# Optimization experiments

Measured on AMD Instinct MI355X. Metric: run time of the kernel, lower is better.

The kernel has to match this reference:

```python
import jax, jax.numpy as jnp
import numpy as np

B, S, E, H = 2, 2048, 1024, 16
D = E // H  # head dim = 64


def setup_inputs() -> dict:
    key = jax.random.key(0)
    ks = jax.random.split(key, 6)
    x = jax.random.normal(ks[0], (B, S, E), dtype=jnp.float32)
    attn_mask = jax.random.bernoulli(ks[1], 0.1, (B, S, S))  # True = masked
    scale = 1.0 / np.sqrt(E)
    w_kernel = jax.random.normal(ks[2], (E, 3 * E), dtype=jnp.float32) * scale
    w_bias = jax.random.normal(ks[3], (3 * E,), dtype=jnp.float32) * 0.02
    fc_kernel = jax.random.normal(ks[4], (E, E), dtype=jnp.float32) * scale
    fc_bias = jax.random.normal(ks[5], (E,), dtype=jnp.float32) * 0.02
    return {"x": x, "attn_mask": attn_mask, "w_kernel": w_kernel,
            "w_bias": w_bias, "fc_kernel": fc_kernel, "fc_bias": fc_bias}


def reference(x, attn_mask, w_kernel, w_bias, fc_kernel, fc_bias):
    b, s, e = x.shape
    qkv = jnp.einsum("bse,ef->bsf", x, w_kernel) + w_bias  # (B,S,3E)
    q, k, v = jnp.split(qkv, 3, axis=-1)

    def heads(t):  # (B,S,E) -> (B,H,S,D)
        return t.reshape(b, s, H, D).transpose(0, 2, 1, 3)

    q, k, v = heads(q), heads(k), heads(v)
    scores = jnp.einsum("bhqd,bhkd->bhqk", q, k) / jnp.sqrt(jnp.float32(D))
    # faithful quirk: masked positions are filled with 1e-9, not -inf
    scores = jnp.where(attn_mask[:, None, :, :], jnp.float32(1e-9), scores)
    A = jax.nn.softmax(scores, axis=-1)
    out = jnp.einsum("bhqk,bhkd->bhqd", A, v)  # (B,H,S,D)
    out = out.transpose(0, 2, 1, 3).reshape(b, s, e)
    # dropout is identity in eval mode
    return jnp.einsum("bse,ef->bsf", out, fc_kernel) + fc_bias
```

## Files before the change

### kernel.cpp

```cpp
#include <hip/hip_runtime.h>
#include <math.h>

#define BB 2
#define SS 2048
#define EE 1024
#define HH 16

typedef _Float16 f16;
typedef __attribute__((ext_vector_type(8))) _Float16 f16x8;
typedef __attribute__((ext_vector_type(4))) _Float16 f16x4;
typedef __attribute__((ext_vector_type(4))) float f32x4;

__global__ __launch_bounds__(256) void cvt_f32_f16(
    const float* __restrict__ in, f16* __restrict__ out, int n)
{
  int i = (blockIdx.x * 256 + threadIdx.x) * 8;
  if (i >= n) return;
  float4 a = *(const float4*)(in + i);
  float4 b = *(const float4*)(in + i + 4);
  f16x8 o;
  o[0] = (f16)a.x; o[1] = (f16)a.y; o[2] = (f16)a.z; o[3] = (f16)a.w;
  o[4] = (f16)b.x; o[5] = (f16)b.y; o[6] = (f16)b.z; o[7] = (f16)b.w;
  *(f16x8*)(out + i) = o;
}

__global__ __launch_bounds__(256) void transpose_cvt(
    const float* __restrict__ in, f16* __restrict__ out, int K, int N)
{
  __shared__ float T[64][65];
  const int k0 = blockIdx.y * 64, n0 = blockIdx.x * 64;
  const int tr = threadIdx.x >> 4, tc = (threadIdx.x & 15) * 4;
#pragma unroll
  for (int i = 0; i < 4; ++i) {
    int r = tr + i * 16;
    *(float4*)&T[r][tc] = *(const float4*)(in + (size_t)(k0 + r) * N + n0 + tc);
  }
  __syncthreads();
#pragma unroll
  for (int i = 0; i < 4; ++i) {
    int nl = tr + i * 16;
    f16x4 v;
    v[0] = (f16)T[tc + 0][nl];
    v[1] = (f16)T[tc + 1][nl];
    v[2] = (f16)T[tc + 2][nl];
    v[3] = (f16)T[tc + 3][nl];
    *(f16x4*)(out + (size_t)(n0 + nl) * K + k0 + tc) = v;
  }
}

__global__ __launch_bounds__(256) void pack_mask(
    const int* __restrict__ m, unsigned long long* __restrict__ bits)
{
  const int i = blockIdx.x * 256 + threadIdx.x;
  const unsigned long long bal = __ballot(m[i] != 0);
  if ((threadIdx.x & 63) == 0) bits[i >> 6] = bal;
}

__global__ __launch_bounds__(256) void gemm_f16(
    const f16* __restrict__ A, const f16* __restrict__ Bt,
    const float* __restrict__ bias, int M, int N, int K, int mode,
    f16* __restrict__ oQK, f16* __restrict__ oVT, float* __restrict__ oF32)
{
  __shared__ f16 Ah[128][36];
  __shared__ f16 Bh[128][36];

  const int t = threadIdx.x;
  const int l = t & 63, w = t >> 6;
  const int l15 = l & 15, l4 = l >> 4;
  const int wr = w >> 1, wc = w & 1;
  const int n0 = blockIdx.x * 128, m0 = blockIdx.y * 128;

  const int srow = t >> 1, soff = (t & 1) * 16;
  const f16* Ap = A + (size_t)(m0 + srow) * K + soff;
  const f16* Bp = Bt + (size_t)(n0 + srow) * K + soff;

  f32x4 acc[4][4] = {};

  f16x8 ra0 = *(const f16x8*)(Ap);
  f16x8 ra1 = *(const f16x8*)(Ap + 8);
  f16x8 rb0 = *(const f16x8*)(Bp);
  f16x8 rb1 = *(const f16x8*)(Bp + 8);

  for (int k0 = 0; k0 < K; k0 += 32) {
    __syncthreads();
    *(f16x8*)&Ah[srow][soff]     = ra0;
    *(f16x8*)&Ah[srow][soff + 8] = ra1;
    *(f16x8*)&Bh[srow][soff]     = rb0;
    *(f16x8*)&Bh[srow][soff + 8] = rb1;
    __syncthreads();
    if (k0 + 32 < K) {
      ra0 = *(const f16x8*)(Ap + k0 + 32);
      ra1 = *(const f16x8*)(Ap + k0 + 40);
      rb0 = *(const f16x8*)(Bp + k0 + 32);
      rb1 = *(const f16x8*)(Bp + k0 + 40);
    }
    f16x8 af[4], bf[4];
#pragma unroll
    for (int mr = 0; mr < 4; ++mr)
      af[mr] = *(const f16x8*)&Ah[wr * 64 + mr * 16 + l15][l4 * 8];
#pragma unroll
    for (int nr = 0; nr < 4; ++nr)
      bf[nr] = *(const f16x8*)&Bh[wc * 64 + nr * 16 + l15][l4 * 8];
#pragma unroll
    for (int mr = 0; mr < 4; ++mr)
#pragma unroll
      for (int nr = 0; nr < 4; ++nr)
        acc[mr][nr] = __builtin_amdgcn_mfma_f32_16x16x32_f16(
            af[mr], bf[nr], acc[mr][nr], 0, 0, 0);
  }

  if (mode == 1) {
#pragma unroll
    for (int nr = 0; nr < 4; ++nr) {
      const int n = n0 + wc * 64 + nr * 16 + l15;
      const float bv = bias[n];
#pragma unroll
      for (int mr = 0; mr < 4; ++mr)
#pragma unroll
        for (int j = 0; j < 4; ++j) {
          const int m = m0 + wr * 64 + mr * 16 + l4 * 4 + j;
          oF32[(size_t)m * N + n] = acc[mr][nr][j] + bv;
        }
    }
  } else {
#pragma unroll
    for (int nr = 0; nr < 4; ++nr) {
      const int n = n0 + wc * 64 + nr * 16 + l15;
      const float bv = bias[n];
      if (n < 2048) {
#pragma unroll
        for (int mr = 0; mr < 4; ++mr)
#pragma unroll
          for (int j = 0; j < 4; ++j) {
            const int m = m0 + wr * 64 + mr * 16 + l4 * 4 + j;
            oQK[(size_t)m * 2048 + n] = (f16)(acc[mr][nr][j] + bv);
          }
      } else {
        const int hh = (n - 2048) >> 6;
        const int d = (n - 2048) & 63;
#pragma unroll
        for (int mr = 0; mr < 4; ++mr) {
          const int tok0 = m0 + wr * 64 + mr * 16 + l4 * 4;
          const int bq = tok0 >> 11, sq = tok0 & 2047;
          f16x4 v;
          v[0] = (f16)(acc[mr][nr][0] + bv);
          v[1] = (f16)(acc[mr][nr][1] + bv);
          v[2] = (f16)(acc[mr][nr][2] + bv);
          v[3] = (f16)(acc[mr][nr][3] + bv);
          *(f16x4*)(oVT + ((size_t)(bq * 16 + hh) * 64 + d) * SS + sq) = v;
        }
      }
    }
  }
}

__global__ __launch_bounds__(256, 2) void attn_mfma(
    const f16* __restrict__ qkbuf, const f16* __restrict__ vT,
    const unsigned long long* __restrict__ mbits, f16* __restrict__ aout)
{
  __shared__ f16 Kds[2][64 * 64];
  __shared__ f16 Vds[2][64 * 64];

  const int t = threadIdx.x;
  const int w = t >> 6, l = t & 63, l15 = l & 15, l4 = l >> 4;
  const int bh = blockIdx.y, b = bh >> 4, h = bh & 15;
  const int qbase = blockIdx.x * 128 + w * 32;

  f16x8 q00, q01, q10, q11;
  {
    const size_t r0 = (size_t)(b * SS + qbase + l15) * 2048 + h * 64;
    const size_t r1 = (size_t)(b * SS + qbase + 16 + l15) * 2048 + h * 64;
    q00 = *(const f16x8*)(qkbuf + r0 + l4 * 8);
    q01 = *(const f16x8*)(qkbuf + r0 + 32 + l4 * 8);
    q10 = *(const f16x8*)(qkbuf + r1 + l4 * 8);
    q11 = *(const f16x8*)(qkbuf + r1 + 32 + l4 * 8);
  }

  f32x4 accA[4] = {}, accB[4] = {};
  float lsA = 0.f, lsB = 0.f;

  const unsigned long long* mA = mbits + (size_t)(b * SS + qbase + l15) * 32;
  const unsigned long long* mB = mbits + (size_t)(b * SS + qbase + 16 + l15) * 32;

  const int srow = t >> 3;
  const int scb  = (t & 7) * 8;
  const int sws  = (srow & 7) << 3;
  const f16* kb = qkbuf + (size_t)b * SS * 2048 + 1024 + h * 64 + scb;
  const f16* vb = vT + ((size_t)bh * 64 + srow) * SS + scb;

  f16x8 kr0, kr1, vr0, vr1;
#define LOADT(kt)                                                         \
  {                                                                       \
    kr0 = *(const f16x8*)(kb + (size_t)((kt) + srow) * 2048);             \
    kr1 = *(const f16x8*)(kb + (size_t)((kt) + srow + 32) * 2048);        \
    vr0 = *(const f16x8*)(vb + (kt));                                     \
    vr1 = *(const f16x8*)(vb + 32 * SS + (kt));                           \
  }
#define COMMIT(bi)                                                        \
  {                                                                       \
    *(f16x8*)&Kds[bi][srow * 64 + (scb ^ sws)]        = kr0;              \
    *(f16x8*)&Kds[bi][(srow + 32) * 64 + (scb ^ sws)] = kr1;              \
    *(f16x8*)&Vds[bi][srow * 64 + (scb ^ sws)]        = vr0;              \
    *(f16x8*)&Vds[bi][(srow + 32) * 64 + (scb ^ sws)] = vr1;              \
  }

  LOADT(0)
  COMMIT(0)
  LOADT(64)
  __syncthreads();

  const int swr = (l15 & 7) << 3;

  for (int tI = 0; tI < 32; ++tI) {
    const int cur = tI & 1;
    const unsigned long long mbA = mA[tI];
    const unsigned long long mbB = mB[tI];

#pragma unroll
    for (int g = 0; g < 4; ++g) {
      const f16* krow = &Kds[cur][(g * 16 + l15) * 64];
      const f16x8 k0 = *(const f16x8*)(krow + ((l4 * 8) ^ swr));
      const f16x8 k1 = *(const f16x8*)(krow + ((32 + l4 * 8) ^ swr));
      f32x4 SA = __builtin_amdgcn_mfma_f32_16x16x32_f16(
          k0, q00, (f32x4){0.f, 0.f, 0.f, 0.f}, 0, 0, 0);
      SA = __builtin_amdgcn_mfma_f32_16x16x32_f16(k1, q01, SA, 0, 0, 0);
      f32x4 SB = __builtin_amdgcn_mfma_f32_16x16x32_f16(
          k0, q10, (f32x4){0.f, 0.f, 0.f, 0.f}, 0, 0, 0);
      SB = __builtin_amdgcn_mfma_f32_16x16x32_f16(k1, q11, SB, 0, 0, 0);

      const unsigned int nibA = (unsigned int)(mbA >> (g * 16 + l4 * 4));
      const unsigned int nibB = (unsigned int)(mbB >> (g * 16 + l4 * 4));
      f16x4 paA, paB;
#pragma unroll
      for (int j = 0; j < 4; ++j) {
        const float pA = ((nibA >> j) & 1u) ? 1.0f : __expf(SA[j] * 0.125f);
        const float pB = ((nibB >> j) & 1u) ? 1.0f : __expf(SB[j] * 0.125f);
        lsA += pA;
        lsB += pB;
        paA[j] = (f16)pA;
        paB[j] = (f16)pB;
      }
#pragma unroll
      for (int dg = 0; dg < 4; ++dg) {
        const f16x4 vf = *(const f16x4*)&Vds[cur][(dg * 16 + l15) * 64 +
                                                  ((g * 16 + l4 * 4) ^ swr)];
        accA[dg] = __builtin_amdgcn_mfma_f32_16x16x16f16(paA, vf, accA[dg], 0, 0, 0);
        accB[dg] = __builtin_amdgcn_mfma_f32_16x16x16f16(paB, vf, accB[dg], 0, 0, 0);
      }
    }

    if (tI + 1 < 32) {
      COMMIT(cur ^ 1)
      if (tI + 2 < 32) LOADT((tI + 2) * 64)
    }
    __syncthreads();
  }

  lsA += __shfl_xor(lsA, 16);
  lsA += __shfl_xor(lsA, 32);
  lsB += __shfl_xor(lsB, 16);
  lsB += __shfl_xor(lsB, 32);

#pragma unroll
  for (int j = 0; j < 4; ++j) {
    const int qr = l4 * 4 + j;
    const float invA = 1.0f / __shfl(lsA, qr);
    const float invB = 1.0f / __shfl(lsB, qr);
    const size_t rowA = (size_t)(b * SS + qbase + qr) * EE + h * 64 + l15;
    const size_t rowB = (size_t)(b * SS + qbase + 16 + qr) * EE + h * 64 + l15;
#pragma unroll
    for (int dg = 0; dg < 4; ++dg) {
      aout[rowA + dg * 16] = (f16)(accA[dg][j] * invA);
      aout[rowB + dg * 16] = (f16)(accB[dg][j] * invB);
    }
  }
}

extern "C" void kernel_launch(void* const* d_in, const int* in_sizes, int n_in,
                              void* d_out, int out_size, void* d_ws,
                              size_t ws_size, hipStream_t stream)
{
  (void)in_sizes; (void)n_in; (void)out_size; (void)ws_size;
  const float* x   = (const float*)d_in[0];
  const int* mask  = (const int*)d_in[1];
  const float* wk  = (const float*)d_in[2];
  const float* wb  = (const float*)d_in[3];
  const float* fck = (const float*)d_in[4];
  const float* fcb = (const float*)d_in[5];
  float* out       = (float*)d_out;

  char* ws = (char*)d_ws;
  size_t off = 0;
  f16* xh    = (f16*)(ws + off); off += (size_t)4096 * 1024 * 2;
  f16* Wt    = (f16*)(ws + off); off += (size_t)3072 * 1024 * 2;
  f16* fckT  = (f16*)(ws + off); off += (size_t)1024 * 1024 * 2;
  f16* qk    = (f16*)(ws + off); off += (size_t)4096 * 2048 * 2;
  f16* vT    = (f16*)(ws + off); off += (size_t)BB * HH * 64 * SS * 2;
  f16* aoutH = (f16*)(ws + off); off += (size_t)4096 * 1024 * 2;
  unsigned long long* mbits = (unsigned long long*)(ws + off);
  off += (size_t)BB * SS * SS / 8;

  cvt_f32_f16<<<4096 * 1024 / (8 * 256), 256, 0, stream>>>(x, xh, 4096 * 1024);
  transpose_cvt<<<dim3(3072 / 64, 1024 / 64), 256, 0, stream>>>(wk, Wt, 1024, 3072);
  transpose_cvt<<<dim3(1024 / 64, 1024 / 64), 256, 0, stream>>>(fck, fckT, 1024, 1024);
  pack_mask<<<BB * SS * SS / 256, 256, 0, stream>>>(mask, mbits);

  gemm_f16<<<dim3(3072 / 128, 4096 / 128), 256, 0, stream>>>(
      xh, Wt, wb, 4096, 3072, 1024, 0, qk, vT, nullptr);

  attn_mfma<<<dim3(SS / 128, BB * HH), 256, 0, stream>>>(qk, vT, mbits, aoutH);

  gemm_f16<<<dim3(1024 / 128, 4096 / 128), 256, 0, stream>>>(
      aoutH, fckT, fcb, 4096, 1024, 1024, 1, nullptr, nullptr, out);
}
```

Before: 243.6 us.

## Use direct global-to-LDS loads in GEMM and streamline attention softmax with exp2 and MFMA rowsums

The GEMM now loads tiles straight from global memory into swizzled LDS with global_load_lds, replacing the register-staged double buffer. In attention, Q is pre-scaled by log2(e)/sqrt(D) in the GEMM epilogue so the softmax can use a bare exp2. Probabilities are packed with cvt_pkrtz into the wider 16x16x32 MFMA, row sums are computed by an MFMA against a ones vector instead of scalar adds and shuffles, and mask words are prefetched one tile ahead. The GEMM loses its register prefetch overlap, and round-toward-zero packing slightly changes numerics.

```diff
diff --git a/kernel.cpp b/kernel.cpp
--- a/kernel.cpp
+++ b/kernel.cpp
@@ -9,7 +9,33 @@
 typedef _Float16 f16;
 typedef __attribute__((ext_vector_type(8))) _Float16 f16x8;
 typedef __attribute__((ext_vector_type(4))) _Float16 f16x4;
+typedef __attribute__((ext_vector_type(2))) _Float16 f16x2;
 typedef __attribute__((ext_vector_type(4))) float f32x4;
+
+union P8 { f16x8 v8; f16x2 h2[4]; };
+union V8 { f16x8 v8; f16x4 v4[2]; };
+
+#define QSCALE 0.18033688011112042f
+
+#if __has_builtin(__builtin_amdgcn_exp2f)
+#define EXP2(x) __builtin_amdgcn_exp2f(x)
+#else
+#define EXP2(x) exp2f(x)
+#endif
+
+static __device__ __forceinline__ f16x2 pk2(float a, float b) {
+#if __has_builtin(__builtin_amdgcn_cvt_pkrtz)
+  return __builtin_bit_cast(f16x2, __builtin_amdgcn_cvt_pkrtz(a, b));
+#else
+  f16x2 r; r[0] = (f16)a; r[1] = (f16)b; return r;
+#endif
+}
+
+static __device__ __forceinline__ void gl16(const void* g, void* l) {
+  __builtin_amdgcn_global_load_lds(
+      (const __attribute__((address_space(1))) void*)g,
+      (__attribute__((address_space(3))) void*)l, 16, 0, 0);
+}
 
 __global__ __launch_bounds__(256) void cvt_f32_f16(
     const float* __restrict__ in, f16* __restrict__ out, int n)
@@ -61,8 +87,8 @@
     const float* __restrict__ bias, int M, int N, int K, int mode,
     f16* __restrict__ oQK, f16* __restrict__ oVT, float* __restrict__ oF32)
 {
-  __shared__ f16 Ah[128][36];
-  __shared__ f16 Bh[128][36];
+  __shared__ f16 Ah[128 * 32];
+  __shared__ f16 Bh[128 * 32];
 
   const int t = threadIdx.x;
   const int l = t & 63, w = t >> 6;
@@ -70,43 +96,45 @@
   const int wr = w >> 1, wc = w & 1;
   const int n0 = blockIdx.x * 128, m0 = blockIdx.y * 128;
 
-  const int srow = t >> 1, soff = (t & 1) * 16;
-  const f16* Ap = A + (size_t)(m0 + srow) * K + soff;
-  const f16* Bp = Bt + (size_t)(n0 + srow) * K + soff;
+  const int srow = l >> 2;
+  const int gch  = (l & 3) ^ (srow & 3);
+  const f16* Ap0 = A + (size_t)(m0 + w * 32 + srow) * K + gch * 8;
+  const f16* Ap1 = Ap0 + (size_t)16 * K;
+  const f16* Bp0 = Bt + (size_t)(n0 + w * 32 + srow) * K + gch * 8;
+  const f16* Bp1 = Bp0 + (size_t)16 * K;
+  f16* ldsA0 = &Ah[(w * 32) * 32];
+  f16* ldsA1 = &Ah[(w * 32 + 16) * 32];
+  f16* ldsB0 = &Bh[(w * 32) * 32];
+  f16* ldsB1 = &Bh[(w * 32 + 16) * 32];
 
   f32x4 acc[4][4] = {};
-
-  f16x8 ra0 = *(const f16x8*)(Ap);
-  f16x8 ra1 = *(const f16x8*)(Ap + 8);
-  f16x8 rb0 = *(const f16x8*)(Bp);
-  f16x8 rb1 = *(const f16x8*)(Bp + 8);
+  const int csw = (l15 & 3);
 
   for (int k0 = 0; k0 < K; k0 += 32) {
+    gl16(Ap0 + k0, ldsA0);
+    gl16(Ap1 + k0, ldsA1);
+    gl16(Bp0 + k0, ldsB0);
+    gl16(Bp1 + k0, ldsB1);
     __syncthreads();
-    *(f16x8*)&Ah[srow][soff]     = ra0;
-    *(f16x8*)&Ah[srow][soff + 8] = ra1;
-    *(f16x8*)&Bh[srow][soff]     = rb0;
-    *(f16x8*)&Bh[srow][soff + 8] = rb1;
-    __syncthreads();
-    if (k0 + 32 < K) {
-      ra0 = *(const f16x8*)(Ap + k0 + 32);
-      ra1 = *(const f16x8*)(Ap + k0 + 40);
-      rb0 = *(const f16x8*)(Bp + k0 + 32);
-      rb1 = *(const f16x8*)(Bp + k0 + 40);
-    }
+
     f16x8 af[4], bf[4];
 #pragma unroll
-    for (int mr = 0; mr < 4; ++mr)
-      af[mr] = *(const f16x8*)&Ah[wr * 64 + mr * 16 + l15][l4 * 8];
-#pragma unroll
-    for (int nr = 0; nr < 4; ++nr)
-      bf[nr] = *(const f16x8*)&Bh[wc * 64 + nr * 16 + l15][l4 * 8];
+    for (int mr = 0; mr < 4; ++mr) {
+      const int row = wr * 64 + mr * 16 + l15;
+      af[mr] = *(const f16x8*)&Ah[row * 32 + ((l4 ^ csw) * 8)];
+    }
+#pragma unroll
+    for (int nr = 0; nr < 4; ++nr) {
+      const int row = wc * 64 + nr * 16 + l15;
+      bf[nr] = *(const f16x8*)&Bh[row * 32 + ((l4 ^ csw) * 8)];
+    }
 #pragma unroll
     for (int mr = 0; mr < 4; ++mr)
 #pragma unroll
       for (int nr = 0; nr < 4; ++nr)
         acc[mr][nr] = __builtin_amdgcn_mfma_f32_16x16x32_f16(
             af[mr], bf[nr], acc[mr][nr], 0, 0, 0);
+    __syncthreads();
   }
 
   if (mode == 1) {
@@ -128,12 +156,13 @@
       const int n = n0 + wc * 64 + nr * 16 + l15;
       const float bv = bias[n];
       if (n < 2048) {
+        const float qs = (n < 1024) ? QSCALE : 1.0f;
 #pragma unroll
         for (int mr = 0; mr < 4; ++mr)
 #pragma unroll
           for (int j = 0; j < 4; ++j) {
             const int m = m0 + wr * 64 + mr * 16 + l4 * 4 + j;
-            oQK[(size_t)m * 2048 + n] = (f16)(acc[mr][nr][j] + bv);
+            oQK[(size_t)m * 2048 + n] = (f16)((acc[mr][nr][j] + bv) * qs);
           }
       } else {
         const int hh = (n - 2048) >> 6;
@@ -177,7 +206,10 @@
   }
 
   f32x4 accA[4] = {}, accB[4] = {};
-  float lsA = 0.f, lsB = 0.f;
+  f32x4 accLA = {}, accLB = {};
+  f16x8 ones;
+#pragma unroll
+  for (int i = 0; i < 8; ++i) ones[i] = (f16)1.0f;
 
   const unsigned long long* mA = mbits + (size_t)(b * SS + qbase + l15) * 32;
   const unsigned long long* mB = mbits + (size_t)(b * SS + qbase + 16 + l15) * 32;
@@ -211,42 +243,54 @@
 
   const int swr = (l15 & 7) << 3;
 
+  unsigned long long mbA = mA[0], mbB = mB[0];
+
   for (int tI = 0; tI < 32; ++tI) {
     const int cur = tI & 1;
-    const unsigned long long mbA = mA[tI];
-    const unsigned long long mbB = mB[tI];
-
-#pragma unroll
-    for (int g = 0; g < 4; ++g) {
-      const f16* krow = &Kds[cur][(g * 16 + l15) * 64];
-      const f16x8 k0 = *(const f16x8*)(krow + ((l4 * 8) ^ swr));
-      const f16x8 k1 = *(const f16x8*)(krow + ((32 + l4 * 8) ^ swr));
-      f32x4 SA = __builtin_amdgcn_mfma_f32_16x16x32_f16(
-          k0, q00, (f32x4){0.f, 0.f, 0.f, 0.f}, 0, 0, 0);
-      SA = __builtin_amdgcn_mfma_f32_16x16x32_f16(k1, q01, SA, 0, 0, 0);
-      f32x4 SB = __builtin_amdgcn_mfma_f32_16x16x32_f16(
-          k0, q10, (f32x4){0.f, 0.f, 0.f, 0.f}, 0, 0, 0);
-      SB = __builtin_amdgcn_mfma_f32_16x16x32_f16(k1, q11, SB, 0, 0, 0);
-
-      const unsigned int nibA = (unsigned int)(mbA >> (g * 16 + l4 * 4));
-      const unsigned int nibB = (unsigned int)(mbB >> (g * 16 + l4 * 4));
-      f16x4 paA, paB;
-#pragma unroll
-      for (int j = 0; j < 4; ++j) {
-        const float pA = ((nibA >> j) & 1u) ? 1.0f : __expf(SA[j] * 0.125f);
-        const float pB = ((nibB >> j) & 1u) ? 1.0f : __expf(SB[j] * 0.125f);
-        lsA += pA;
-        lsB += pB;
-        paA[j] = (f16)pA;
-        paB[j] = (f16)pB;
+    unsigned long long nmbA = 0, nmbB = 0;
+    if (tI + 1 < 32) { nmbA = mA[tI + 1]; nmbB = mB[tI + 1]; }
+
+#pragma unroll
+    for (int sg = 0; sg < 2; ++sg) {
+      float pA[8], pB[8];
+#pragma unroll
+      for (int gh = 0; gh < 2; ++gh) {
+        const int g = sg * 2 + gh;
+        const f16* krow = &Kds[cur][(g * 16 + l15) * 64];
+        const f16x8 k0 = *(const f16x8*)(krow + ((l4 * 8) ^ swr));
+        const f16x8 k1 = *(const f16x8*)(krow + ((32 + l4 * 8) ^ swr));
+        f32x4 SA = __builtin_amdgcn_mfma_f32_16x16x32_f16(
+            k0, q00, (f32x4){0.f, 0.f, 0.f, 0.f}, 0, 0, 0);
+        SA = __builtin_amdgcn_mfma_f32_16x16x32_f16(k1, q01, SA, 0, 0, 0);
+        f32x4 SB = __builtin_amdgcn_mfma_f32_16x16x32_f16(
+            k0, q10, (f32x4){0.f, 0.f, 0.f, 0.f}, 0, 0, 0);
+        SB = __builtin_amdgcn_mfma_f32_16x16x32_f16(k1, q11, SB, 0, 0, 0);
+
+        const unsigned int nibA = (unsigned int)(mbA >> (g * 16 + l4 * 4));
+        const unsigned int nibB = (unsigned int)(mbB >> (g * 16 + l4 * 4));
+#pragma unroll
+        for (int j = 0; j < 4; ++j) {
+          pA[gh * 4 + j] = ((nibA >> j) & 1u) ? 1.0f : EXP2(SA[j]);
+          pB[gh * 4 + j] = ((nibB >> j) & 1u) ? 1.0f : EXP2(SB[j]);
+        }
       }
+      P8 uA, uB;
+      uA.h2[0] = pk2(pA[0], pA[1]); uA.h2[1] = pk2(pA[2], pA[3]);
+      uA.h2[2] = pk2(pA[4], pA[5]); uA.h2[3] = pk2(pA[6], pA[7]);
+      uB.h2[0] = pk2(pB[0], pB[1]); uB.h2[1] = pk2(pB[2], pB[3]);
+      uB.h2[2] = pk2(pB[4], pB[5]); uB.h2[3] = pk2(pB[6], pB[7]);
+
 #pragma unroll
       for (int dg = 0; dg < 4; ++dg) {
-        const f16x4 vf = *(const f16x4*)&Vds[cur][(dg * 16 + l15) * 64 +
-                                                  ((g * 16 + l4 * 4) ^ swr)];
-        accA[dg] = __builtin_amdgcn_mfma_f32_16x16x16f16(paA, vf, accA[dg], 0, 0, 0);
-        accB[dg] = __builtin_amdgcn_mfma_f32_16x16x16f16(paB, vf, accB[dg], 0, 0, 0);
+        const f16* vrow = &Vds[cur][(dg * 16 + l15) * 64];
+        V8 uv;
+        uv.v4[0] = *(const f16x4*)(vrow + ((sg * 32 + l4 * 4) ^ swr));
+        uv.v4[1] = *(const f16x4*)(vrow + ((sg * 32 + 16 + l4 * 4) ^ swr));
+        accA[dg] = __builtin_amdgcn_mfma_f32_16x16x32_f16(uA.v8, uv.v8, accA[dg], 0, 0, 0);
+        accB[dg] = __builtin_amdgcn_mfma_f32_16x16x32_f16(uB.v8, uv.v8, accB[dg], 0, 0, 0);
       }
+      accLA = __builtin_amdgcn_mfma_f32_16x16x32_f16(uA.v8, ones, accLA, 0, 0, 0);
+      accLB = __builtin_amdgcn_mfma_f32_16x16x32_f16(uB.v8, ones, accLB, 0, 0, 0);
     }
 
     if (tI + 1 < 32) {
@@ -254,18 +298,14 @@
       if (tI + 2 < 32) LOADT((tI + 2) * 64)
     }
     __syncthreads();
-  }
-
-  lsA += __shfl_xor(lsA, 16);
-  lsA += __shfl_xor(lsA, 32);
-  lsB += __shfl_xor(lsB, 16);
-  lsB += __shfl_xor(lsB, 32);
+    mbA = nmbA; mbB = nmbB;
+  }
 
 #pragma unroll
   for (int j = 0; j < 4; ++j) {
     const int qr = l4 * 4 + j;
-    const float invA = 1.0f / __shfl(lsA, qr);
-    const float invB = 1.0f / __shfl(lsB, qr);
+    const float invA = 1.0f / accLA[j];
+    const float invB = 1.0f / accLB[j];
     const size_t rowA = (size_t)(b * SS + qbase + qr) * EE + h * 64 + l15;
     const size_t rowB = (size_t)(b * SS + qbase + 16 + qr) * EE + h * 64 + l15;
 #pragma unroll
```

After: 240.2 us. No clear change (-1.4%).
